# Kernel tuning notes

Hardware: AMD Instinct MI355X
Metric: run time of the kernel (lower is better)

## Reference

```python
import jax, jax.numpy as jnp
import numpy as np

B, N, DS, DP, H, DH, DFF = 1, 1024, 768, 128, 16, 48, 1536


def _ln(x, eps=1e-5):
    m = jnp.mean(x, axis=-1, keepdims=True)
    v = jnp.var(x, axis=-1, keepdims=True)
    return (x - m) * jax.lax.rsqrt(v + eps)


def _ada_ln(a, s, gw, gb, bw):
    # AF3-style adaptive layernorm: sigmoid(Linear(LN(s))) * LN(a) + Linear(LN(s))
    sn = _ln(s)
    return jax.nn.sigmoid(sn @ gw + gb) * _ln(a) + sn @ bw


def setup_inputs() -> dict:
    key = jax.random.key(0)
    ks = jax.random.split(key, 24)
    w = lambda k, shape: jax.random.normal(k, shape, dtype=jnp.float32) * 0.02
    return {
        'x': jax.random.normal(ks[0], (B, N, DS), dtype=jnp.float32),
        'single_cond': jax.random.normal(ks[1], (B, N, DS), dtype=jnp.float32),
        'pair_cond': jax.random.normal(ks[2], (B, N, N, DP), dtype=jnp.float32),
        'attn_gamma_w': w(ks[3], (DS, DS)), 'attn_gamma_b': jnp.zeros((DS,), jnp.float32),
        'attn_beta_w': w(ks[4], (DS, DS)),
        'wq': w(ks[5], (DS, H * DH)), 'bq': jnp.zeros((H * DH,), jnp.float32),
        'wk': w(ks[6], (DS, H * DH)), 'wv': w(ks[7], (DS, H * DH)),
        'wb': w(ks[8], (DP, H)),
        'wg': w(ks[9], (DS, H * DH)),
        'wo': w(ks[10], (H * DH, DS)),
        'attn_gate_w': w(ks[11], (DS, DS)), 'attn_gate_b': jnp.full((DS,), -2.0, jnp.float32),
        'ff_gamma_w': w(ks[12], (DS, DS)), 'ff_gamma_b': jnp.zeros((DS,), jnp.float32),
        'ff_beta_w': w(ks[13], (DS, DS)),
        'ff_w1': w(ks[14], (DS, DFF)), 'ff_w2': w(ks[15], (DS, DFF)),
        'ff_w3': w(ks[16], (DFF, DS)),
        'ff_gate_w': w(ks[17], (DS, DS)), 'ff_gate_b': jnp.full((DS,), -2.0, jnp.float32),
        'mask': jnp.ones((B, N), dtype=bool),
    }


def reference(x, single_cond, pair_cond, attn_gamma_w, attn_gamma_b, attn_beta_w,
              wq, bq, wk, wv, wb, wg, wo, attn_gate_w, attn_gate_b,
              ff_gamma_w, ff_gamma_b, ff_beta_w, ff_w1, ff_w2, ff_w3,
              ff_gate_w, ff_gate_b, mask):
    # --- AttentionPairBias (edge bias + cond adaLN + gated output) ---
    a = _ada_ln(x, single_cond, attn_gamma_w, attn_gamma_b, attn_beta_w)
    q = (a @ wq + bq).reshape(B, N, H, DH)  # q has bias (q_use_bias=True)
    k = (a @ wk).reshape(B, N, H, DH)
    v = (a @ wv).reshape(B, N, H, DH)
    bias = jnp.einsum('bijp,ph->bhij', _ln(pair_cond), wb)  # pair bias per head
    logits = jnp.einsum('bihd,bjhd->bhij', q, k) * (1.0 / np.float32(np.sqrt(DH))) + bias
    logits = jnp.where(mask[:, None, None, :], logits, jnp.float32(-1e9))
    attn = jax.nn.softmax(logits, axis=-1)
    o = jnp.einsum('bhij,bjhd->bihd', attn, v)
    g = jax.nn.sigmoid(a @ wg).reshape(B, N, H, DH)  # gating (g_use_bias=False)
    attn_out = (g * o).reshape(B, N, H * DH) @ wo  # o_use_bias=False
    attn_out = jax.nn.sigmoid(single_cond @ attn_gate_w + attn_gate_b) * attn_out
    # --- ConditionedFeedForward (adaLN + SwiGLU + cond output gate) ---
    f = _ada_ln(x, single_cond, ff_gamma_w, ff_gamma_b, ff_beta_w)
    h = jax.nn.silu(f @ ff_w1) * (f @ ff_w2)
    ff_out = jax.nn.sigmoid(single_cond @ ff_gate_w + ff_gate_b) * (h @ ff_w3)
    # dropout p=0 (eval) -> identity; residual add of both branches
    return x + attn_out + ff_out
```

## Files before the change

kernel.cpp:

```cpp
#include <hip/hip_runtime.h>
#include <hip/hip_bf16.h>


typedef __attribute__((ext_vector_type(8))) short bf16x8;
typedef __attribute__((ext_vector_type(4))) float f32x4;
typedef __attribute__((ext_vector_type(4))) unsigned short us4;

#define DEVFN static __device__ __forceinline__

DEVFN float bf2f(unsigned short u){
  union { unsigned int u; float f; } v; v.u = ((unsigned int)u) << 16; return v.f;
}
DEVFN unsigned short f2bf(float f){
  union { float f; unsigned int u; } v; v.f = f;
  unsigned int r = v.u + 0x7fffu + ((v.u >> 16) & 1u);
  return (unsigned short)(r >> 16);
}
DEVFN float sigf(float x){ return 1.f / (1.f + __expf(-x)); }

DEVFN void gload16(const void* g, void* l){
  __builtin_amdgcn_global_load_lds(
      (const __attribute__((address_space(1))) void*)g,
      (__attribute__((address_space(3))) void*)l, 16, 0, 0);
}

#define OFF_SN    0x0000000ULL
#define OFF_SC    0x0180000ULL
#define OFF_XA    0x0300000ULL
#define OFF_W1    0x0600000ULL
#define OFF_W2    0x0A80000ULL
#define OFF_W3    0x0CC0000ULL
#define OFF_W4    0x1140000ULL
#define OFF_W5    0x15C0000ULL
#define OFF_W6    0x1800000ULL
#define OFF_BIAS1 0x1920000ULL
#define OFF_BIASG 0x1923000ULL
#define OFF_BIASQ 0x1924800ULL
#define OFF_G1    0x1930000ULL
#define OFF_GATES 0x2530000ULL
#define OFF_A     0x2B30000ULL
#define OFF_F     0x2CB0000ULL
#define OFF_QKVG  0x2E30000ULL
#define OFF_VT    0x3430000ULL
#define OFF_HH    0x4030000ULL
#define OFF_GO    0x4330000ULL
#define OFF_PB    0x47B0000ULL

struct WJobs {
  const float* src[14];
  unsigned long long dst[14];
  int K[14];
  int N[14];
  int rowmul[14];
  int rowoff[14];
};

__global__ __launch_bounds__(256) void transpose_cast_kernel(WJobs jobs, char* ws){
  const int z = blockIdx.z;
  const int n0 = blockIdx.x * 32, k0 = blockIdx.y * 32;
  const int K = jobs.K[z], N = jobs.N[z];
  if(n0 >= N || k0 >= K) return;
  __shared__ float t[32][33];
  const int tx = threadIdx.x, ty = threadIdx.y;
  const float* src = jobs.src[z];
  #pragma unroll
  for(int i=0;i<4;i++)
    t[ty + i*8][tx] = src[(long long)(k0 + ty + i*8) * N + n0 + tx];
  __syncthreads();
  unsigned short* dst = (unsigned short*)(ws + jobs.dst[z]);
  const int rm = jobs.rowmul[z], ro = jobs.rowoff[z];
  #pragma unroll
  for(int i=0;i<4;i++)
    dst[(long long)((n0 + ty + i*8)*rm + ro) * K + k0 + tx] = f2bf(t[tx][ty + i*8]);
}

__global__ __launch_bounds__(256) void ln_kernel(const float* __restrict__ x,
    const float* __restrict__ sc, unsigned short* __restrict__ sn_bf,
    unsigned short* __restrict__ sc_bf, float* __restrict__ xa,
    const float* agb, const float* bq, const float* gtb, const float* fgtb,
    const float* fgb, float* bias1, float* biasg, float* biasq){
  if(blockIdx.x >= 1024){
    int t = (blockIdx.x - 1024) * 256 + threadIdx.x;
    float v = 0.f;
    if(t < 768) v = agb[t];
    else if(t >= 1536 && t < 2304) v = fgb[t - 1536];
    bias1[t] = v;
    biasq[t] = (t < 768) ? bq[t] : 0.f;
    if(t < 1536) biasg[t] = (t < 768) ? gtb[t] : fgtb[t - 768];
    return;
  }
  const int row = blockIdx.x, t = threadIdx.x;
  const float* xr = x + (long long)row * 768;
  const float* sr = sc + (long long)row * 768;
  float xs[3], ss[3];
  float s0=0.f, s1=0.f, s2=0.f, s3=0.f;
  #pragma unroll
  for(int i=0;i<3;i++){
    float xv = xr[t + i*256], sv = sr[t + i*256];
    xs[i]=xv; ss[i]=sv;
    s0 += xv; s1 += xv*xv; s2 += sv; s3 += sv*sv;
  }
  #pragma unroll
  for(int o=32;o;o>>=1){
    s0 += __shfl_xor(s0,o); s1 += __shfl_xor(s1,o);
    s2 += __shfl_xor(s2,o); s3 += __shfl_xor(s3,o);
  }
  __shared__ float red[4][4];
  const int w = t >> 6;
  if((t & 63) == 0){ red[0][w]=s0; red[1][w]=s1; red[2][w]=s2; red[3][w]=s3; }
  __syncthreads();
  float tx0 = red[0][0]+red[0][1]+red[0][2]+red[0][3];
  float tx1 = red[1][0]+red[1][1]+red[1][2]+red[1][3];
  float ts0 = red[2][0]+red[2][1]+red[2][2]+red[2][3];
  float ts1 = red[3][0]+red[3][1]+red[3][2]+red[3][3];
  const float inv = 1.f/768.f;
  float mx = tx0*inv, vx = tx1*inv - mx*mx;
  float ms = ts0*inv, vs = ts1*inv - ms*ms;
  float rsx = rsqrtf(vx + 1e-5f), rss = rsqrtf(vs + 1e-5f);
  #pragma unroll
  for(int i=0;i<3;i++){
    int c = t + i*256;
    xa[(long long)row*768 + c]    = (xs[i]-mx)*rsx;
    sn_bf[(long long)row*768 + c] = f2bf((ss[i]-ms)*rss);
    sc_bf[(long long)row*768 + c] = f2bf(ss[i]);
  }
}

DEVFN void gemm_tile_f32(const unsigned short* __restrict__ A,
                         const unsigned short* __restrict__ Bt,
                         int N, int K, int m0, int n0,
                         const float* __restrict__ bias,
                         float* __restrict__ Cf, int epi,
                         unsigned short* sA, unsigned short* sB, int tid){
  const int w = tid >> 6, l = tid & 63, l15 = l & 15, l4 = l >> 4;
  const int wm = w >> 1, wn = w & 1;
  f32x4 zf = {0.f,0.f,0.f,0.f};
  f32x4 acc[4][4];
  #pragma unroll
  for(int m=0;m<4;m++)
    #pragma unroll
    for(int n=0;n<4;n++) acc[m][n] = zf;

  const int srow = w*16 + (l >> 2);
  const int scol = (l & 3) * 8;
  const unsigned short* gA = A  + (long long)(m0 + srow) * K + scol;
  const unsigned short* gB = Bt + (long long)(n0 + srow) * K + scol;
  unsigned short* lA0 = &sA[(w*16)*32];
  unsigned short* lA1 = &sA[(64 + w*16)*32];
  unsigned short* lB0 = &sB[(w*16)*32];
  unsigned short* lB1 = &sB[(64 + w*16)*32];
  const long long half = (long long)64 * K;

  for(int k0 = 0; k0 < K; k0 += 32){
    gload16(gA + k0, lA0);
    gload16(gA + half + k0, lA1);
    gload16(gB + k0, lB0);
    gload16(gB + half + k0, lB1);
    __syncthreads();
    bf16x8 af[4], bg[4];
    #pragma unroll
    for(int m=0;m<4;m++) af[m] = *(const bf16x8*)&sA[(wm*64 + m*16 + l15)*32 + l4*8];
    #pragma unroll
    for(int n=0;n<4;n++) bg[n] = *(const bf16x8*)&sB[(wn*64 + n*16 + l15)*32 + l4*8];
    #pragma unroll
    for(int m=0;m<4;m++)
      #pragma unroll
      for(int n=0;n<4;n++)
        acc[m][n] = __builtin_amdgcn_mfma_f32_16x16x32_bf16(af[m], bg[n], acc[m][n], 0, 0, 0);
    __syncthreads();
  }
  #pragma unroll
  for(int m=0;m<4;m++){
    #pragma unroll
    for(int n=0;n<4;n++){
      #pragma unroll
      for(int r=0;r<4;r++){
        const int i = m0 + wm*64 + m*16 + l4*4 + r;
        const int c = n0 + wn*64 + n*16 + l15;
        float v = acc[m][n][r] + bias[c];
        Cf[(long long)i*N + c] = epi ? sigf(v) : v;
      }
    }
  }
}

__global__ __launch_bounds__(256) void fused1_kernel(
    const float* __restrict__ pair, const float* __restrict__ wb,
    unsigned short* __restrict__ pb,
    const unsigned short* __restrict__ SN, const unsigned short* __restrict__ W1,
    const float* __restrict__ B1, float* __restrict__ G1,
    const unsigned short* __restrict__ SC, const unsigned short* __restrict__ W2,
    const float* __restrict__ BG, float* __restrict__ GT){
  __shared__ unsigned short sA[128*32];
  __shared__ unsigned short sB[128*32];
  const int bid = blockIdx.x;
  const int tid = threadIdx.x;
  const bool isg = (bid % 15) == 0;
  if(isg){
    const int jb = bid / 15;
    if(jb >= 288) return;
    if(jb < 192){
      gemm_tile_f32(SN, W1, 3072, 768, (jb & 7)*128, (jb >> 3)*128, B1, G1, 0, sA, sB, tid);
    } else {
      const int t = jb - 192;
      gemm_tile_f32(SC, W2, 1536, 768, (t & 7)*128, (t >> 3)*128, BG, GT, 1, sA, sB, tid);
    }
    return;
  }
  const int pbid = bid - (bid/15 + 1);
  const int l = tid & 63, w = tid >> 6, l15 = l & 15, l4 = l >> 4;
  bf16x8 wbf[4];
  #pragma unroll
  for(int c=0;c<4;c++){
    bf16x8 t;
    #pragma unroll
    for(int e=0;e<8;e++) t[e] = (short)f2bf(wb[(c*32 + l4*8 + e)*16 + l15]);
    wbf[c] = t;
  }
  f32x4 zf = {0.f,0.f,0.f,0.f};
  #pragma unroll
  for(int q=0;q<4;q++){
    const long long tile = (long long)pbid * 16 + q*4 + w;
    const long long row0 = tile << 4;
    const float* pr = pair + ((row0 + l15) << 7);
    float vals[32];
    #pragma unroll
    for(int c=0;c<4;c++){
      float4 v0 = *(const float4*)(pr + c*32 + l4*8);
      float4 v1 = *(const float4*)(pr + c*32 + l4*8 + 4);
      vals[c*8+0]=v0.x; vals[c*8+1]=v0.y; vals[c*8+2]=v0.z; vals[c*8+3]=v0.w;
      vals[c*8+4]=v1.x; vals[c*8+5]=v1.y; vals[c*8+6]=v1.z; vals[c*8+7]=v1.w;
    }
    float s=0.f, s2=0.f;
    #pragma unroll
    for(int e=0;e<32;e++){ s += vals[e]; s2 += vals[e]*vals[e]; }
    s += __shfl_xor(s, 16); s2 += __shfl_xor(s2, 16);
    s += __shfl_xor(s, 32); s2 += __shfl_xor(s2, 32);
    const float m = s * (1.f/128.f);
    const float rs = rsqrtf(s2*(1.f/128.f) - m*m + 1e-5f);
    f32x4 acc = zf;
    #pragma unroll
    for(int c=0;c<4;c++){
      bf16x8 af;
      #pragma unroll
      for(int e=0;e<8;e++) af[e] = (short)f2bf((vals[c*8+e] - m) * rs);
      acc = __builtin_amdgcn_mfma_f32_16x16x32_bf16(af, wbf[c], acc, 0,0,0);
    }
    us4 o;
    #pragma unroll
    for(int r=0;r<4;r++) o[r] = f2bf(acc[r]);
    *(us4*)&pb[((long long)l15 << 20) + row0 + l4*4] = o;
  }
}

__global__ __launch_bounds__(256) void ew1_kernel(const float* __restrict__ g1,
    const float* __restrict__ xa, unsigned short* __restrict__ a_bf,
    unsigned short* __restrict__ f_bf, const float* __restrict__ x,
    float* __restrict__ out){
  const int i = blockIdx.x;
  const int c = blockIdx.y * 256 + threadIdx.x;
  const float* row = g1 + (long long)i * 3072;
  float xv = xa[(long long)i*768 + c];
  a_bf[(long long)i*768 + c] = f2bf(sigf(row[c])      * xv + row[768 + c]);
  f_bf[(long long)i*768 + c] = f2bf(sigf(row[1536+c]) * xv + row[2304 + c]);
  out[(long long)i*768 + c] = x[(long long)i*768 + c];
}

__global__ __launch_bounds__(256) void fused2_kernel(
    const unsigned short* __restrict__ A_, const unsigned short* __restrict__ W3,
    const float* __restrict__ BQ, unsigned short* __restrict__ QKVG,
    unsigned short* __restrict__ VT,
    const unsigned short* __restrict__ F_, const unsigned short* __restrict__ W4,
    unsigned short* __restrict__ HH){
  __shared__ unsigned short sA[128*32];
  __shared__ unsigned short sB[128*32];
  const int jb = blockIdx.x;
  const int tid = threadIdx.x;
  const bool isq = jb < 192;
  const int t = isq ? jb : jb - 192;
  const int m0 = (t & 7) * 128, n0 = (t >> 3) * 128;
  const unsigned short* A  = isq ? A_ : F_;
  const unsigned short* Bt = isq ? W3 : W4;
  const int K = 768;

  const int w = tid >> 6, l = tid & 63, l15 = l & 15, l4 = l >> 4;
  const int wm = w >> 1, wn = w & 1;
  f32x4 zf = {0.f,0.f,0.f,0.f};
  f32x4 acc[4][4];
  #pragma unroll
  for(int m=0;m<4;m++)
    #pragma unroll
    for(int n=0;n<4;n++) acc[m][n] = zf;

  const int srow = w*16 + (l >> 2);
  const int scol = (l & 3) * 8;
  const unsigned short* gA = A  + (long long)(m0 + srow) * K + scol;
  const unsigned short* gB = Bt + (long long)(n0 + srow) * K + scol;
  unsigned short* lA0 = &sA[(w*16)*32];
  unsigned short* lA1 = &sA[(64 + w*16)*32];
  unsigned short* lB0 = &sB[(w*16)*32];
  unsigned short* lB1 = &sB[(64 + w*16)*32];
  const long long half = (long long)64 * K;

  for(int k0 = 0; k0 < K; k0 += 32){
    gload16(gA + k0, lA0);
    gload16(gA + half + k0, lA1);
    gload16(gB + k0, lB0);
    gload16(gB + half + k0, lB1);
    __syncthreads();
    bf16x8 af[4], bg[4];
    #pragma unroll
    for(int m=0;m<4;m++) af[m] = *(const bf16x8*)&sA[(wm*64 + m*16 + l15)*32 + l4*8];
    #pragma unroll
    for(int n=0;n<4;n++) bg[n] = *(const bf16x8*)&sB[(wn*64 + n*16 + l15)*32 + l4*8];
    #pragma unroll
    for(int m=0;m<4;m++)
      #pragma unroll
      for(int n=0;n<4;n++)
        acc[m][n] = __builtin_amdgcn_mfma_f32_16x16x32_bf16(af[m], bg[n], acc[m][n], 0, 0, 0);
    __syncthreads();
  }
  if(isq){
    #pragma unroll
    for(int m=0;m<4;m++){
      #pragma unroll
      for(int n=0;n<4;n++){
        const int c = n0 + wn*64 + n*16 + l15;
        const int ibase = m0 + wm*64 + m*16 + l4*4;
        unsigned short vb[4];
        #pragma unroll
        for(int r=0;r<4;r++){
          vb[r] = f2bf(acc[m][n][r] + BQ[c]);
          QKVG[(long long)(ibase + r)*3072 + c] = vb[r];
        }
        if(c >= 1536 && c < 2304){
          us4 o; o.x=vb[0]; o.y=vb[1]; o.z=vb[2]; o.w=vb[3];
          *(us4*)&VT[((long long)(c - 1536) << 10) + ibase] = o;
        }
      }
    }
  } else {
    #pragma unroll
    for(int m=0;m<4;m++){
      #pragma unroll
      for(int n=0;n<4;n++){
        #pragma unroll
        for(int r=0;r<4;r++){
          const int i = m0 + wm*64 + m*16 + l4*4 + r;
          const int c = n0 + wn*64 + n*16 + l15;
          float v = acc[m][n][r];
          float partner = __shfl_xor(v, 1);
          if((c & 1) == 0)
            HH[(long long)i*1536 + (c>>1)] = f2bf(v * sigf(v) * partner);
        }
      }
    }
  }
}

__global__ __launch_bounds__(256) void attn_kernel(
    const unsigned short* __restrict__ qkvg,
    const unsigned short* __restrict__ pbias,
    const unsigned short* __restrict__ VT,
    unsigned short* __restrict__ go){
  const int h  = blockIdx.x >> 6;
  const int i0 = (blockIdx.x & 63) << 4;
  const int tid = threadIdx.x;
  const int w = tid >> 6, l = tid & 63, l15 = l & 15, l4 = l >> 4;

  __shared__ unsigned short sP[16][1032];
  __shared__ float sRedM[16][4];
  __shared__ float sRedS[16][4];
  __shared__ float sO[4][16][48];

  f32x4 zf = {0.f,0.f,0.f,0.f};
  bf16x8 zero8 = {0,0,0,0,0,0,0,0};

  const unsigned short* pbh = pbias + ((long long)h << 20) + ((long long)i0 << 10);
  #pragma unroll
  for(int it=0; it<8; it++){
    const int idx = it*2048 + tid*8;
    const int r = idx >> 10, c = idx & 1023;
    *(bf16x8*)&sP[r][c] = *(const bf16x8*)&pbh[((long long)r << 10) + c];
  }

  f32x4 accs[16];
  #pragma unroll
  for(int f=0;f<16;f++) accs[f] = zf;
  bf16x8 aq0, aq1;
  {
    const unsigned short* qp = qkvg + (long long)(i0 + l15)*3072 + h*48;
    aq0 = *(const bf16x8*)(qp + l4*8);
    aq1 = *(const bf16x8*)(qp + 32 + l4*8);
  }
  const int jbase = w * 256;
  #pragma unroll
  for(int f=0; f<16; f++){
    const int j = jbase + f*16 + l15;
    const unsigned short* kp = qkvg + (long long)j*3072 + 768 + h*48;
    bf16x8 bk0 = *(const bf16x8*)(kp + l4*8);
    bf16x8 bk1 = *(const bf16x8*)(kp + 32 + l4*8);
    if(l4 >= 2) bk1 = zero8;
    accs[f] = __builtin_amdgcn_mfma_f32_16x16x32_bf16(aq0, bk0, accs[f], 0,0,0);
    accs[f] = __builtin_amdgcn_mfma_f32_16x16x32_bf16(aq1, bk1, accs[f], 0,0,0);
  }
  __syncthreads();

  const float scale = 0.14433756729740643f;
  #pragma unroll
  for(int f=0;f<16;f++){
    #pragma unroll
    for(int r=0;r<4;r++)
      accs[f][r] = accs[f][r]*scale + bf2f(sP[l4*4 + r][jbase + f*16 + l15]);
  }
  float pm[4];
  #pragma unroll
  for(int r=0;r<4;r++){
    float m = accs[0][r];
    #pragma unroll
    for(int f=1;f<16;f++) m = fmaxf(m, accs[f][r]);
    #pragma unroll
    for(int o=1;o<16;o<<=1) m = fmaxf(m, __shfl_xor(m, o));
    pm[r] = m;
  }
  if(l15 == 0){
    #pragma unroll
    for(int r=0;r<4;r++) sRedM[l4*4 + r][w] = pm[r];
  }
  __syncthreads();
  float rowm[4];
  #pragma unroll
  for(int r=0;r<4;r++){
    const int i = l4*4 + r;
    rowm[r] = fmaxf(fmaxf(sRedM[i][0], sRedM[i][1]), fmaxf(sRedM[i][2], sRedM[i][3]));
  }
  float psum[4] = {0.f,0.f,0.f,0.f};
  #pragma unroll
  for(int f=0;f<16;f++)
    #pragma unroll
    for(int r=0;r<4;r++){
      float p = __expf(accs[f][r] - rowm[r]);
      accs[f][r] = p;
      psum[r] += p;
    }
  #pragma unroll
  for(int r=0;r<4;r++)
    #pragma unroll
    for(int o=1;o<16;o<<=1) psum[r] += __shfl_xor(psum[r], o);
  if(l15 == 0){
    #pragma unroll
    for(int r=0;r<4;r++) sRedS[l4*4 + r][w] = psum[r];
  }
  #pragma unroll
  for(int f=0;f<16;f++)
    #pragma unroll
    for(int r=0;r<4;r++)
      sP[l4*4 + r][jbase + f*16 + l15] = f2bf(accs[f][r]);

  f32x4 acco[3];
  #pragma unroll
  for(int n=0;n<3;n++) acco[n] = zf;
  const unsigned short* vth = VT + ((long long)(h*48) << 10);
  #pragma unroll
  for(int c=0; c<4; c++){
    const int jb = jbase + c*64;
    #pragma unroll
    for(int kk=0; kk<2; kk++){
      bf16x8 pa = *(const bf16x8*)&sP[l15][jb + kk*32 + l4*8];
      #pragma unroll
      for(int n=0;n<3;n++){
        bf16x8 bv = *(const bf16x8*)&vth[((long long)(n*16 + l15) << 10) + jb + kk*32 + l4*8];
        acco[n] = __builtin_amdgcn_mfma_f32_16x16x32_bf16(pa, bv, acco[n], 0,0,0);
      }
    }
  }
  #pragma unroll
  for(int n=0;n<3;n++)
    #pragma unroll
    for(int r=0;r<4;r++)
      sO[w][l4*4 + r][n*16 + l15] = acco[n][r];
  __syncthreads();
  for(int t = tid; t < 768; t += 256){
    const int i = t / 48, d = t % 48;
    float o = sO[0][i][d] + sO[1][i][d] + sO[2][i][d] + sO[3][i][d];
    float lsum = sRedS[i][0] + sRedS[i][1] + sRedS[i][2] + sRedS[i][3];
    float gv = bf2f(qkvg[(long long)(i0 + i)*3072 + 2304 + h*48 + d]);
    go[(long long)(i0 + i)*768 + h*48 + d] = f2bf(sigf(gv) * (o / lsum));
  }
}

__global__ __launch_bounds__(256) void final_kernel(
    const unsigned short* __restrict__ GO, const unsigned short* __restrict__ W6t,
    const unsigned short* __restrict__ HH, const unsigned short* __restrict__ W5t,
    const float* __restrict__ gates, float* __restrict__ out){
  __shared__ unsigned short sA[128*32];
  __shared__ unsigned short sB[128*32];
  const int m0 = blockIdx.x * 128, n0 = blockIdx.y * 128;
  const int z = blockIdx.z;
  const bool pA = z < 4;
  const unsigned short* A  = pA ? GO  : HH;
  const unsigned short* Bt = pA ? W6t : W5t;
  const int K    = pA ? 768 : 1536;
  const int kbeg = pA ? z*192 : (z-4)*384;
  const int kend = pA ? kbeg + 192 : kbeg + 384;
  const int goff = pA ? 0 : 768;
  const int tid = threadIdx.x;
  const int w = tid >> 6, l = tid & 63, l15 = l & 15, l4 = l >> 4;
  const int wm = w >> 1, wn = w & 1;
  f32x4 zf = {0.f,0.f,0.f,0.f};
  f32x4 acc[4][4];
  #pragma unroll
  for(int m=0;m<4;m++)
    #pragma unroll
    for(int n=0;n<4;n++) acc[m][n] = zf;

  const int srow = w*16 + (l >> 2);
  const int scol = (l & 3) * 8;
  const unsigned short* gA = A  + (long long)(m0 + srow) * K + scol;
  const unsigned short* gB = Bt + (long long)(n0 + srow) * K + scol;
  unsigned short* lA0 = &sA[(w*16)*32];
  unsigned short* lA1 = &sA[(64 + w*16)*32];
  unsigned short* lB0 = &sB[(w*16)*32];
  unsigned short* lB1 = &sB[(64 + w*16)*32];
  const long long half = (long long)64 * K;

  for(int k0 = kbeg; k0 < kend; k0 += 32){
    gload16(gA + k0, lA0);
    gload16(gA + half + k0, lA1);
    gload16(gB + k0, lB0);
    gload16(gB + half + k0, lB1);
    __syncthreads();
    bf16x8 af[4], bg[4];
    #pragma unroll
    for(int m=0;m<4;m++) af[m] = *(const bf16x8*)&sA[(wm*64 + m*16 + l15)*32 + l4*8];
    #pragma unroll
    for(int n=0;n<4;n++) bg[n] = *(const bf16x8*)&sB[(wn*64 + n*16 + l15)*32 + l4*8];
    #pragma unroll
    for(int m=0;m<4;m++)
      #pragma unroll
      for(int n=0;n<4;n++)
        acc[m][n] = __builtin_amdgcn_mfma_f32_16x16x32_bf16(af[m], bg[n], acc[m][n], 0, 0, 0);
    __syncthreads();
  }
  #pragma unroll
  for(int m=0;m<4;m++){
    #pragma unroll
    for(int n=0;n<4;n++){
      #pragma unroll
      for(int r=0;r<4;r++){
        const int i = m0 + wm*64 + m*16 + l4*4 + r;
        const int c = n0 + wn*64 + n*16 + l15;
        float v = gates[(long long)i*1536 + goff + c] * acc[m][n][r];
        __hip_atomic_fetch_add(&out[(long long)i*768 + c], v,
                               __ATOMIC_RELAXED, __HIP_MEMORY_SCOPE_AGENT);
      }
    }
  }
}

extern "C" void kernel_launch(void* const* d_in, const int* in_sizes, int n_in,
                              void* d_out, int out_size, void* d_ws, size_t ws_size,
                              hipStream_t stream){
  (void)in_sizes; (void)n_in; (void)out_size; (void)ws_size;
  const float* x    = (const float*)d_in[0];
  const float* sc   = (const float*)d_in[1];
  const float* pair = (const float*)d_in[2];
  const float* agw  = (const float*)d_in[3];
  const float* agb  = (const float*)d_in[4];
  const float* abw  = (const float*)d_in[5];
  const float* wq   = (const float*)d_in[6];
  const float* bq   = (const float*)d_in[7];
  const float* wk   = (const float*)d_in[8];
  const float* wv   = (const float*)d_in[9];
  const float* wb   = (const float*)d_in[10];
  const float* wg   = (const float*)d_in[11];
  const float* wo   = (const float*)d_in[12];
  const float* gtw  = (const float*)d_in[13];
  const float* gtb  = (const float*)d_in[14];
  const float* fgw  = (const float*)d_in[15];
  const float* fgb  = (const float*)d_in[16];
  const float* fbw  = (const float*)d_in[17];
  const float* fw1  = (const float*)d_in[18];
  const float* fw2  = (const float*)d_in[19];
  const float* fw3  = (const float*)d_in[20];
  const float* fgtw = (const float*)d_in[21];
  const float* fgtb = (const float*)d_in[22];
  float* out = (float*)d_out;
  char* ws = (char*)d_ws;

  unsigned short* SN   = (unsigned short*)(ws + OFF_SN);
  unsigned short* SC   = (unsigned short*)(ws + OFF_SC);
  float*          XA   = (float*)(ws + OFF_XA);
  unsigned short* W1   = (unsigned short*)(ws + OFF_W1);
  unsigned short* W2   = (unsigned short*)(ws + OFF_W2);
  unsigned short* W3   = (unsigned short*)(ws + OFF_W3);
  unsigned short* W4   = (unsigned short*)(ws + OFF_W4);
  unsigned short* W5   = (unsigned short*)(ws + OFF_W5);
  unsigned short* W6   = (unsigned short*)(ws + OFF_W6);
  float*          B1   = (float*)(ws + OFF_BIAS1);
  float*          BG   = (float*)(ws + OFF_BIASG);
  float*          BQ   = (float*)(ws + OFF_BIASQ);
  float*          G1   = (float*)(ws + OFF_G1);
  float*          GT   = (float*)(ws + OFF_GATES);
  unsigned short* A_   = (unsigned short*)(ws + OFF_A);
  unsigned short* F_   = (unsigned short*)(ws + OFF_F);
  unsigned short* QKVG = (unsigned short*)(ws + OFF_QKVG);
  unsigned short* VT   = (unsigned short*)(ws + OFF_VT);
  unsigned short* HH   = (unsigned short*)(ws + OFF_HH);
  unsigned short* GO   = (unsigned short*)(ws + OFF_GO);
  unsigned short* PB   = (unsigned short*)(ws + OFF_PB);

  WJobs jobs;
  int ji = 0;
  auto setj = [&](const float* s, unsigned long long off, int K, int N,
                  int rm = 1, int ro = 0){
    jobs.src[ji]=s; jobs.dst[ji]=off; jobs.K[ji]=K; jobs.N[ji]=N;
    jobs.rowmul[ji]=rm; jobs.rowoff[ji]=ro; ji++;
  };
  const unsigned long long W768 = 768ULL*768ULL*2ULL;
  setj(agw,  OFF_W1 + 0*W768, 768, 768);
  setj(abw,  OFF_W1 + 1*W768, 768, 768);
  setj(fgw,  OFF_W1 + 2*W768, 768, 768);
  setj(fbw,  OFF_W1 + 3*W768, 768, 768);
  setj(gtw,  OFF_W2 + 0*W768, 768, 768);
  setj(fgtw, OFF_W2 + 1*W768, 768, 768);
  setj(wq,   OFF_W3 + 0*W768, 768, 768);
  setj(wk,   OFF_W3 + 1*W768, 768, 768);
  setj(wv,   OFF_W3 + 2*W768, 768, 768);
  setj(wg,   OFF_W3 + 3*W768, 768, 768);
  setj(fw1,  OFF_W4, 768, 1536, 2, 0);
  setj(fw2,  OFF_W4, 768, 1536, 2, 1);
  setj(fw3,  OFF_W5, 1536, 768);
  setj(wo,   OFF_W6, 768, 768);

  transpose_cast_kernel<<<dim3(48,48,14), dim3(32,8), 0, stream>>>(jobs, ws);
  ln_kernel<<<1036, 256, 0, stream>>>(x, sc, SN, SC, XA,
      agb, bq, gtb, fgtb, fgb, B1, BG, BQ);
  fused1_kernel<<<4389, 256, 0, stream>>>(pair, wb, PB,
      SN, W1, B1, G1, SC, W2, BG, GT);
  ew1_kernel<<<dim3(1024,3), 256, 0, stream>>>(G1, XA, A_, F_, x, out);
  fused2_kernel<<<384, 256, 0, stream>>>(A_, W3, BQ, QKVG, VT, F_, W4, HH);
  attn_kernel<<<1024, 256, 0, stream>>>(QKVG, PB, VT, GO);
  final_kernel<<<dim3(8,6,8), 256, 0, stream>>>(GO, W6, HH, W5, GT, out);
}
```

Baseline: 277.5 us.

## Merge transpose and LN launches; split pair-bias work across two GEMM kernels

The weight transpose-cast and layernorm kernels are merged into one prep launch, using a flat block index that walks the job list. The pair-bias projection, previously interleaved with the first GEMM kernel, is split in half. The first 2048 blocks run alongside the adaLN GEMMs and the remaining 2048 run alongside the QKVG/FFN GEMMs. The aim is to cut launch count and fill idle CUs during the small GEMM phases with the memory-bound pair-LN work, at the cost of a serial job-search loop per transpose block.

```diff
diff --git a/kernel.cpp b/kernel.cpp
--- a/kernel.cpp
+++ b/kernel.cpp
@@ -55,32 +55,40 @@
   int rowoff[14];
 };
 
-__global__ __launch_bounds__(256) void transpose_cast_kernel(WJobs jobs, char* ws){
-  const int z = blockIdx.z;
-  const int n0 = blockIdx.x * 32, k0 = blockIdx.y * 32;
-  const int K = jobs.K[z], N = jobs.N[z];
-  if(n0 >= N || k0 >= K) return;
-  __shared__ float t[32][33];
-  const int tx = threadIdx.x, ty = threadIdx.y;
-  const float* src = jobs.src[z];
-  #pragma unroll
-  for(int i=0;i<4;i++)
-    t[ty + i*8][tx] = src[(long long)(k0 + ty + i*8) * N + n0 + tx];
-  __syncthreads();
-  unsigned short* dst = (unsigned short*)(ws + jobs.dst[z]);
-  const int rm = jobs.rowmul[z], ro = jobs.rowoff[z];
-  #pragma unroll
-  for(int i=0;i<4;i++)
-    dst[(long long)((n0 + ty + i*8)*rm + ro) * K + k0 + tx] = f2bf(t[tx][ty + i*8]);
-}
-
-__global__ __launch_bounds__(256) void ln_kernel(const float* __restrict__ x,
-    const float* __restrict__ sc, unsigned short* __restrict__ sn_bf,
-    unsigned short* __restrict__ sc_bf, float* __restrict__ xa,
+__global__ __launch_bounds__(256) void prep_kernel(WJobs jobs, char* ws,
+    const float* __restrict__ x, const float* __restrict__ sc,
+    unsigned short* __restrict__ sn_bf, unsigned short* __restrict__ sc_bf,
+    float* __restrict__ xa,
     const float* agb, const float* bq, const float* gtb, const float* fgtb,
     const float* fgb, float* bias1, float* biasg, float* biasq){
-  if(blockIdx.x >= 1024){
-    int t = (blockIdx.x - 1024) * 256 + threadIdx.x;
+  const int bid = blockIdx.x;
+  const int tid = threadIdx.x;
+  if(bid < 9792){
+    int t = bid, z = 0;
+    while(true){
+      int nt = (jobs.N[z] >> 5) * (jobs.K[z] >> 5);
+      if(t < nt) break;
+      t -= nt; z++;
+    }
+    const int nx = jobs.N[z] >> 5;
+    const int n0 = (t % nx) << 5, k0 = (t / nx) << 5;
+    const int K = jobs.K[z], N = jobs.N[z];
+    __shared__ float tt[32][33];
+    const int tx = tid & 31, ty = tid >> 5;
+    const float* src = jobs.src[z];
+    #pragma unroll
+    for(int i=0;i<4;i++)
+      tt[ty + i*8][tx] = src[(long long)(k0 + ty + i*8) * N + n0 + tx];
+    __syncthreads();
+    unsigned short* dst = (unsigned short*)(ws + jobs.dst[z]);
+    const int rm = jobs.rowmul[z], ro = jobs.rowoff[z];
+    #pragma unroll
+    for(int i=0;i<4;i++)
+      dst[(long long)((n0 + ty + i*8)*rm + ro) * K + k0 + tx] = f2bf(tt[tx][ty + i*8]);
+    return;
+  }
+  if(bid >= 10816){
+    int t = (bid - 10816) * 256 + tid;
     float v = 0.f;
     if(t < 768) v = agb[t];
     else if(t >= 1536 && t < 2304) v = fgb[t - 1536];
@@ -89,14 +97,14 @@
     if(t < 1536) biasg[t] = (t < 768) ? gtb[t] : fgtb[t - 768];
     return;
   }
-  const int row = blockIdx.x, t = threadIdx.x;
+  const int row = bid - 9792;
   const float* xr = x + (long long)row * 768;
   const float* sr = sc + (long long)row * 768;
   float xs[3], ss[3];
   float s0=0.f, s1=0.f, s2=0.f, s3=0.f;
   #pragma unroll
   for(int i=0;i<3;i++){
-    float xv = xr[t + i*256], sv = sr[t + i*256];
+    float xv = xr[tid + i*256], sv = sr[tid + i*256];
     xs[i]=xv; ss[i]=sv;
     s0 += xv; s1 += xv*xv; s2 += sv; s3 += sv*sv;
   }
@@ -106,8 +114,8 @@
     s2 += __shfl_xor(s2,o); s3 += __shfl_xor(s3,o);
   }
   __shared__ float red[4][4];
-  const int w = t >> 6;
-  if((t & 63) == 0){ red[0][w]=s0; red[1][w]=s1; red[2][w]=s2; red[3][w]=s3; }
+  const int w = tid >> 6;
+  if((tid & 63) == 0){ red[0][w]=s0; red[1][w]=s1; red[2][w]=s2; red[3][w]=s3; }
   __syncthreads();
   float tx0 = red[0][0]+red[0][1]+red[0][2]+red[0][3];
   float tx1 = red[1][0]+red[1][1]+red[1][2]+red[1][3];
@@ -119,7 +127,7 @@
   float rsx = rsqrtf(vx + 1e-5f), rss = rsqrtf(vs + 1e-5f);
   #pragma unroll
   for(int i=0;i<3;i++){
-    int c = t + i*256;
+    int c = tid + i*256;
     xa[(long long)row*768 + c]    = (xs[i]-mx)*rsx;
     sn_bf[(long long)row*768 + c] = f2bf((ss[i]-ms)*rss);
     sc_bf[(long long)row*768 + c] = f2bf(ss[i]);
@@ -184,7 +192,55 @@
   }
 }
 
-__global__ __launch_bounds__(256) void fused1_kernel(
+DEVFN void pair_block(int pbid, const float* __restrict__ pair,
+                      const float* __restrict__ wb,
+                      unsigned short* __restrict__ pb, int tid){
+  const int l = tid & 63, w = tid >> 6, l15 = l & 15, l4 = l >> 4;
+  bf16x8 wbf[4];
+  #pragma unroll
+  for(int c=0;c<4;c++){
+    bf16x8 t;
+    #pragma unroll
+    for(int e=0;e<8;e++) t[e] = (short)f2bf(wb[(c*32 + l4*8 + e)*16 + l15]);
+    wbf[c] = t;
+  }
+  f32x4 zf = {0.f,0.f,0.f,0.f};
+  #pragma unroll
+  for(int q=0;q<4;q++){
+    const long long tile = (long long)pbid * 16 + q*4 + w;
+    const long long row0 = tile << 4;
+    const float* pr = pair + ((row0 + l15) << 7);
+    float vals[32];
+    #pragma unroll
+    for(int c=0;c<4;c++){
+      float4 v0 = *(const float4*)(pr + c*32 + l4*8);
+      float4 v1 = *(const float4*)(pr + c*32 + l4*8 + 4);
+      vals[c*8+0]=v0.x; vals[c*8+1]=v0.y; vals[c*8+2]=v0.z; vals[c*8+3]=v0.w;
+      vals[c*8+4]=v1.x; vals[c*8+5]=v1.y; vals[c*8+6]=v1.z; vals[c*8+7]=v1.w;
+    }
+    float s=0.f, s2=0.f;
+    #pragma unroll
+    for(int e=0;e<32;e++){ s += vals[e]; s2 += vals[e]*vals[e]; }
+    s += __shfl_xor(s, 16); s2 += __shfl_xor(s2, 16);
+    s += __shfl_xor(s, 32); s2 += __shfl_xor(s2, 32);
+    const float m = s * (1.f/128.f);
+    const float rs = rsqrtf(s2*(1.f/128.f) - m*m + 1e-5f);
+    f32x4 acc = zf;
+    #pragma unroll
+    for(int c=0;c<4;c++){
+      bf16x8 af;
+      #pragma unroll
+      for(int e=0;e<8;e++) af[e] = (short)f2bf((vals[c*8+e] - m) * rs);
+      acc = __builtin_amdgcn_mfma_f32_16x16x32_bf16(af, wbf[c], acc, 0,0,0);
+    }
+    us4 o;
+    #pragma unroll
+    for(int r=0;r<4;r++) o[r] = f2bf(acc[r]);
+    *(us4*)&pb[((long long)l15 << 20) + row0 + l4*4] = o;
+  }
+}
+
+__global__ __launch_bounds__(256) void fA_kernel(
     const float* __restrict__ pair, const float* __restrict__ wb,
     unsigned short* __restrict__ pb,
     const unsigned short* __restrict__ SN, const unsigned short* __restrict__ W1,
@@ -195,62 +251,16 @@
   __shared__ unsigned short sB[128*32];
   const int bid = blockIdx.x;
   const int tid = threadIdx.x;
-  const bool isg = (bid % 15) == 0;
-  if(isg){
-    const int jb = bid / 15;
-    if(jb >= 288) return;
-    if(jb < 192){
-      gemm_tile_f32(SN, W1, 3072, 768, (jb & 7)*128, (jb >> 3)*128, B1, G1, 0, sA, sB, tid);
+  if(bid < 288){
+    if(bid < 192){
+      gemm_tile_f32(SN, W1, 3072, 768, (bid & 7)*128, (bid >> 3)*128, B1, G1, 0, sA, sB, tid);
     } else {
-      const int t = jb - 192;
+      const int t = bid - 192;
       gemm_tile_f32(SC, W2, 1536, 768, (t & 7)*128, (t >> 3)*128, BG, GT, 1, sA, sB, tid);
     }
     return;
   }
-  const int pbid = bid - (bid/15 + 1);
-  const int l = tid & 63, w = tid >> 6, l15 = l & 15, l4 = l >> 4;
-  bf16x8 wbf[4];
-  #pragma unroll
-  for(int c=0;c<4;c++){
-    bf16x8 t;
-    #pragma unroll
-    for(int e=0;e<8;e++) t[e] = (short)f2bf(wb[(c*32 + l4*8 + e)*16 + l15]);
-    wbf[c] = t;
-  }
-  f32x4 zf = {0.f,0.f,0.f,0.f};
-  #pragma unroll
-  for(int q=0;q<4;q++){
-    const long long tile = (long long)pbid * 16 + q*4 + w;
-    const long long row0 = tile << 4;
-    const float* pr = pair + ((row0 + l15) << 7);
-    float vals[32];
-    #pragma unroll
-    for(int c=0;c<4;c++){
-      float4 v0 = *(const float4*)(pr + c*32 + l4*8);
-      float4 v1 = *(const float4*)(pr + c*32 + l4*8 + 4);
-      vals[c*8+0]=v0.x; vals[c*8+1]=v0.y; vals[c*8+2]=v0.z; vals[c*8+3]=v0.w;
-      vals[c*8+4]=v1.x; vals[c*8+5]=v1.y; vals[c*8+6]=v1.z; vals[c*8+7]=v1.w;
-    }
-    float s=0.f, s2=0.f;
-    #pragma unroll
-    for(int e=0;e<32;e++){ s += vals[e]; s2 += vals[e]*vals[e]; }
-    s += __shfl_xor(s, 16); s2 += __shfl_xor(s2, 16);
-    s += __shfl_xor(s, 32); s2 += __shfl_xor(s2, 32);
-    const float m = s * (1.f/128.f);
-    const float rs = rsqrtf(s2*(1.f/128.f) - m*m + 1e-5f);
-    f32x4 acc = zf;
-    #pragma unroll
-    for(int c=0;c<4;c++){
-      bf16x8 af;
-      #pragma unroll
-      for(int e=0;e<8;e++) af[e] = (short)f2bf((vals[c*8+e] - m) * rs);
-      acc = __builtin_amdgcn_mfma_f32_16x16x32_bf16(af, wbf[c], acc, 0,0,0);
-    }
-    us4 o;
-    #pragma unroll
-    for(int r=0;r<4;r++) o[r] = f2bf(acc[r]);
-    *(us4*)&pb[((long long)l15 << 20) + row0 + l4*4] = o;
-  }
+  pair_block(bid - 288, pair, wb, pb, tid);
 }
 
 __global__ __launch_bounds__(256) void ew1_kernel(const float* __restrict__ g1,
@@ -266,7 +276,9 @@
   out[(long long)i*768 + c] = x[(long long)i*768 + c];
 }
 
-__global__ __launch_bounds__(256) void fused2_kernel(
+__global__ __launch_bounds__(256) void fB_kernel(
+    const float* __restrict__ pair, const float* __restrict__ wb,
+    unsigned short* __restrict__ pb,
     const unsigned short* __restrict__ A_, const unsigned short* __restrict__ W3,
     const float* __restrict__ BQ, unsigned short* __restrict__ QKVG,
     unsigned short* __restrict__ VT,
@@ -274,10 +286,14 @@
     unsigned short* __restrict__ HH){
   __shared__ unsigned short sA[128*32];
   __shared__ unsigned short sB[128*32];
-  const int jb = blockIdx.x;
+  const int bid = blockIdx.x;
   const int tid = threadIdx.x;
-  const bool isq = jb < 192;
-  const int t = isq ? jb : jb - 192;
+  if(bid >= 384){
+    pair_block(bid - 384 + 2048, pair, wb, pb, tid);
+    return;
+  }
+  const bool isq = bid < 192;
+  const int t = isq ? bid : bid - 192;
   const int m0 = (t & 7) * 128, n0 = (t >> 3) * 128;
   const unsigned short* A  = isq ? A_ : F_;
   const unsigned short* Bt = isq ? W3 : W4;
@@ -633,13 +649,11 @@
   setj(fw3,  OFF_W5, 1536, 768);
   setj(wo,   OFF_W6, 768, 768);
 
-  transpose_cast_kernel<<<dim3(48,48,14), dim3(32,8), 0, stream>>>(jobs, ws);
-  ln_kernel<<<1036, 256, 0, stream>>>(x, sc, SN, SC, XA,
+  prep_kernel<<<10828, 256, 0, stream>>>(jobs, ws, x, sc, SN, SC, XA,
       agb, bq, gtb, fgtb, fgb, B1, BG, BQ);
-  fused1_kernel<<<4389, 256, 0, stream>>>(pair, wb, PB,
-      SN, W1, B1, G1, SC, W2, BG, GT);
+  fA_kernel<<<2336, 256, 0, stream>>>(pair, wb, PB, SN, W1, B1, G1, SC, W2, BG, GT);
   ew1_kernel<<<dim3(1024,3), 256, 0, stream>>>(G1, XA, A_, F_, x, out);
-  fused2_kernel<<<384, 256, 0, stream>>>(A_, W3, BQ, QKVG, VT, F_, W4, HH);
+  fB_kernel<<<2432, 256, 0, stream>>>(pair, wb, PB, A_, W3, BQ, QKVG, VT, F_, W4, HH);
   attn_kernel<<<1024, 256, 0, stream>>>(QKVG, PB, VT, GO);
   final_kernel<<<dim3(8,6,8), 256, 0, stream>>>(GO, W6, HH, W5, GT, out);
 }
```

Result: no change. 273.7 us (-1.4%).
